# Optimization experiments

Measured on AMD Instinct MI355X. Metric: run time of the kernel, lower is better.

Reference implementation:

```python
import jax, jax.numpy as jnp
import numpy as np

TILE = 16
CLIP_NEAR, CLIP_FAR = 0.01, 10.0


def _sqrt_keepnan(x):
    # forward: sqrt(x) for x>0, NaN otherwise (matches torch.sqrt on negatives);
    # double-where keeps gradients finite.
    pos = x > 0
    return jnp.where(pos, jnp.sqrt(jnp.where(pos, x, 1.0)), jnp.nan)


def _quat_to_rot(q):
    # faithful to the source _quat_to_rot (including its sign quirks)
    x, y, z, w = q[:, 0], q[:, 1], q[:, 2], q[:, 3]
    r0 = jnp.stack([1 - 2 * (y * y + z * z), 2 * (x * y - w * z), 2 * (x * z + w * y)], -1)
    r1 = jnp.stack([2 * (x * y + w * z), 1 - 2 * (x * x - z * z), 2 * (y * z - w * x)], -1)
    r2 = jnp.stack([2 * (x * z + w * y), 2 * (y * z + w * x), 1 - 2 * (x * x + y * y)], -1)
    return jnp.stack([r0, r1, r2], -2)  # (N,3,3)


def _forward(mu, scales, quats, cols, opcs, viewmat, focal, H, W):
    N = mu.shape[0]
    fx = fy = float(focal)
    cx, cy = W / 2.0, H / 2.0
    n_, f_ = CLIP_NEAR, CLIP_FAR

    # --- project gaussians ---
    t = viewmat @ jnp.concatenate([mu.T, jnp.ones((1, N), mu.dtype)], 0)  # (4,N) camera space
    tp0 = (2.0 * fx / W) * t[0]
    tp1 = (2.0 * fy / H) * t[1]
    tp2 = ((f_ + n_) / (f_ - n_)) * t[2] + (-2.0 * f_ * n_ / (f_ - n_)) * t[3]
    tp3 = t[2]
    xys = jnp.stack([W * tp0 / tp3 / 2 + cx, H * tp1 / tp3 / 2 + cy], 1)  # (N,2)
    depths = tp2

    R = _quat_to_rot(quats)
    RS = R * scales[:, None, :]              # R @ diag(s)
    Sigma = RS @ jnp.swapaxes(RS, 1, 2)      # (N,3,3)
    tz = t[2]
    zz = jnp.zeros_like(tz)
    J = jnp.stack([
        jnp.stack([fx / tz, zz, -fx * t[0] / tz ** 2], -1),
        jnp.stack([zz, fy / tz, -fy * t[1] / tz ** 2], -1)], -2)  # (N,2,3)
    Rcw = viewmat[:3, :3]
    M = jnp.einsum('nij,jk->nik', J, Rcw)
    covs = jnp.einsum('nij,njk,nlk->nil', M, Sigma, M)  # (N,2,2)

    ind = jnp.argsort(depths)                # depth sort (front-to-back)
    xys, covs = xys[ind], covs[ind]
    cols_s, opcs_s = cols[ind], opcs[ind]

    # --- bounding boxes -> tile membership mask ---
    a, b, d = covs[:, 0, 0], covs[:, 0, 1], covs[:, 1, 1]
    Aev = jnp.sqrt(a * a - 2 * a * d + 4 * b * b + d * d)
    Bev = a + d
    l1, l2 = 0.5 * (Aev + Bev), 0.5 * (Bev - Aev)
    r1 = 3.0 * _sqrt_keepnan(l1)
    r2 = 3.0 * _sqrt_keepnan(l2)
    mx, my = xys[:, 0], xys[:, 1]
    corners = jnp.stack([
        jnp.stack([mx - r1, my + r2], -1),
        jnp.stack([mx + r1, my + r2], -1),
        jnp.stack([mx + r1, my - r2], -1),
        jnp.stack([mx - r1, my - r2], -1)], 1)  # (N,4,2)
    theta = jnp.where(b != 0, jnp.arctan2(l1 - a, b),
                      jnp.where(a >= d, jnp.pi / 2, 0.0))
    cth, sth = jnp.cos(theta), jnp.sin(theta)
    rot = jnp.stack([jnp.stack([cth, -sth], -1), jnp.stack([sth, cth], -1)], -2)
    bm = corners.mean(1, keepdims=True)
    bbs = jnp.einsum('nij,nkj->nki', rot, corners - bm) + bm
    bbs = jnp.where(jnp.isnan(bbs), -1.0, bbs)
    Wt, Ht = W // TILE, H // TILE
    xmin = jnp.clip(jnp.floor(bbs[:, :, 0].min(1) / TILE), 0, Wt - 1).astype(jnp.int32)
    xmax = jnp.clip(jnp.ceil(bbs[:, :, 0].max(1) / TILE), 0, Wt - 1).astype(jnp.int32)
    ymin = jnp.clip(jnp.floor(bbs[:, :, 1].min(1) / TILE), 0, Ht - 1).astype(jnp.int32)
    ymax = jnp.clip(jnp.ceil(bbs[:, :, 1].max(1) / TILE), 0, Ht - 1).astype(jnp.int32)
    txi = jnp.arange(Wt)
    tyi = jnp.arange(Ht)
    tmask = ((txi[None, None, :] >= xmin[:, None, None]) & (txi[None, None, :] <= xmax[:, None, None]) &
             (tyi[None, :, None] >= ymin[:, None, None]) & (tyi[None, :, None] <= ymax[:, None, None]))  # (N,Ht,Wt)
    pmask = jnp.moveaxis(jnp.repeat(jnp.repeat(tmask, TILE, 1), TILE, 2), 0, -1)  # (H,W,N)

    # --- rasterize: per-pixel gaussian eval + sorted alpha compositing ---
    e = 1e-6
    det = (a + e) * (d + e) - covs[:, 0, 1] * covs[:, 1, 0]
    i00 = (d + e) / det
    i01 = -covs[:, 0, 1] / det
    i10 = -covs[:, 1, 0] / det
    i11 = (a + e) / det
    px = jnp.arange(W, dtype=mu.dtype)
    py = jnp.arange(H, dtype=mu.dtype)
    dx = px[None, :, None] - mx[None, None, :]   # (1,W,N)
    dy = py[:, None, None] - my[None, None, :]   # (H,1,N)
    quad = dx * (i00 * dx + i01 * dy) + dy * (i10 * dx + i11 * dy)  # (H,W,N)
    Pg = jnp.nan_to_num(jnp.exp(-0.5 * quad))
    O = jax.nn.sigmoid(jax.nn.sigmoid(opcs_s))   # double sigmoid: faithful to source
    alpha = O[None, None, :] * Pg
    alpha = jnp.where(pmask, alpha, 0.0)         # only gaussians binned to this tile
    alpha = jnp.where(alpha < 0.001, 0.0, alpha)
    alpha = jnp.minimum(alpha, 0.99)
    trans = jnp.cumprod(1.0 - alpha, -1)         # inclusive transmittance
    Dtr = jnp.concatenate([jnp.ones((H, W, 1), alpha.dtype), trans[..., :-1]], -1)
    C = jnp.clip(cols_s, 1e-4, 1.0)
    rgb = jnp.clip(jnp.einsum('hwn,nc->hwc', alpha * Dtr, C), 1e-4, 1.0)
    nonempty = jnp.repeat(jnp.repeat(tmask.any(0), TILE, 0), TILE, 1)  # empty tiles stay 0
    return jnp.where(nonempty[..., None], rgb, 0.0)


def setup_inputs() -> dict:
    key = jax.random.key(0)
    ks = jax.random.split(key, 6)
    N, H, W = 512, 256, 256
    mu = jax.random.normal(ks[0], (N, 3), jnp.float32)
    scales = jax.random.uniform(ks[1], (N, 3), jnp.float32) * 0.05 + 0.01
    q = jax.random.normal(ks[2], (N, 4), jnp.float32)
    quats = q / jnp.linalg.norm(q, axis=1, keepdims=True)
    cols = jax.random.uniform(ks[3], (N, 3), jnp.float32)
    opcs = jax.random.normal(ks[4], (N,), jnp.float32)
    viewmat = jnp.array([[1, 0, 0, 0], [0, 1, 0, 0], [0, 0, 1, 5.0], [0, 0, 0, 1]], jnp.float32)
    gt = jax.random.uniform(ks[5], (H, W, 3), jnp.float32)
    return {"mu": mu, "scales": scales, "quats": quats, "cols": cols, "opcs": opcs,
            "viewmat": viewmat, "gt": gt, "focal": 200, "H": H, "W": W}


def reference(mu, scales, quats, cols, opcs, viewmat, gt, focal, H, W):
    # gt is accepted (matches source signature) but unused by forward
    return _forward(mu, scales, quats, cols, opcs, viewmat, focal, H, W)
```

## Files before the change

kernel.cpp:

```cpp
#include <hip/hip_runtime.h>
#include <math.h>
#include <float.h>

#define NMAX 512
#define TILE 16
#define FDIV(a,b) __fdividef((a),(b))

__global__ __launch_bounds__(1024) void fused_kernel(
    const float* __restrict__ mu, const float* __restrict__ scales,
    const float* __restrict__ quats, const float* __restrict__ cols,
    const float* __restrict__ opcs, const float* __restrict__ vm,
    const int* __restrict__ focal_p, const int* __restrict__ H_p,
    const int* __restrict__ W_p, float* __restrict__ out, int N)
{
    __shared__ float s_mx[NMAX], s_my[NMAX];
    __shared__ float s_q00[NMAX], s_qs[NMAX], s_q11[NMAX];
    __shared__ float s_O[NMAX], s_c0[NMAX], s_c1[NMAX], s_c2[NMAX];
    __shared__ unsigned long long s_lk[NMAX];
    __shared__ int s_ord[NMAX];
    __shared__ float4 s_part[3][256];
    __shared__ int s_bc[16];

    const int lt = threadIdx.x;
    const int lane = lt & 63, w = lt >> 6;
    const int tx = blockIdx.x, ty = blockIdx.y;

    const int   Wi = W_p[0], Hi = H_p[0];
    const float fx = (float)focal_p[0];
    const float fy = fx;
    const float Wf = (float)Wi, Hf = (float)Hi;
    const float cxf = (float)((double)Wi / 2.0);
    const float cyf = (float)((double)Hi / 2.0);
    const float sxc = (float)(2.0 * (double)fx / (double)Wi);
    const float syc = (float)(2.0 * (double)fy / (double)Hi);
    const float dc1 = (float)((10.0 + 0.01) / (10.0 - 0.01));
    const float dc2 = (float)(-2.0 * 10.0 * 0.01 / (10.0 - 0.01));
    const int Wt = Wi / TILE, Ht = Hi / TILE;

    bool covered = false;
    unsigned int key = 0;
    const int g = lt;
    if (g < N) {
        const float m0 = mu[3*g], m1 = mu[3*g+1], m2 = mu[3*g+2];
        const float t0 = vm[0]*m0  + vm[1]*m1  + vm[2]*m2  + vm[3];
        const float t1 = vm[4]*m0  + vm[5]*m1  + vm[6]*m2  + vm[7];
        const float t2 = vm[8]*m0  + vm[9]*m1  + vm[10]*m2 + vm[11];
        const float t3 = vm[12]*m0 + vm[13]*m1 + vm[14]*m2 + vm[15];

        const float depth = dc1 * t2 + dc2 * t3;
        unsigned int ub = __float_as_uint(depth);
        key = (ub & 0x80000000u) ? ~ub : (ub | 0x80000000u);

        const float mx = FDIV(Wf * (sxc * t0), t2) * 0.5f + cxf;
        const float my = FDIV(Hf * (syc * t1), t2) * 0.5f + cyf;

        const float4 q = ((const float4*)quats)[g];
        const float qx = q.x, qy = q.y, qz = q.z, qw = q.w;
        const float R00 = 1.0f - 2.0f*(qy*qy + qz*qz);
        const float R01 = 2.0f*(qx*qy - qw*qz);
        const float R02 = 2.0f*(qx*qz + qw*qy);
        const float R10 = 2.0f*(qx*qy + qw*qz);
        const float R11 = 1.0f - 2.0f*(qx*qx - qz*qz);
        const float R12 = 2.0f*(qy*qz - qw*qx);
        const float R20 = 2.0f*(qx*qz + qw*qy);
        const float R21 = 2.0f*(qy*qz + qw*qx);
        const float R22 = 1.0f - 2.0f*(qx*qx + qy*qy);

        const float s0 = scales[3*g], s1 = scales[3*g+1], s2 = scales[3*g+2];
        const float A00 = R00*s0, A01 = R01*s1, A02 = R02*s2;
        const float A10 = R10*s0, A11 = R11*s1, A12 = R12*s2;
        const float A20 = R20*s0, A21 = R21*s1, A22 = R22*s2;
        const float S00 = A00*A00 + A01*A01 + A02*A02;
        const float S01 = A00*A10 + A01*A11 + A02*A12;
        const float S02 = A00*A20 + A01*A21 + A02*A22;
        const float S11 = A10*A10 + A11*A11 + A12*A12;
        const float S12 = A10*A20 + A11*A21 + A12*A22;
        const float S22 = A20*A20 + A21*A21 + A22*A22;

        const float tz = t2;
        const float J00 = FDIV(fx, tz);
        const float J02 = FDIV(-fx * t0, tz * tz);
        const float J11 = FDIV(fy, tz);
        const float J12 = FDIV(-fy * t1, tz * tz);
        const float M00 = J00*vm[0] + J02*vm[8];
        const float M01 = J00*vm[1] + J02*vm[9];
        const float M02 = J00*vm[2] + J02*vm[10];
        const float M10 = J11*vm[4] + J12*vm[8];
        const float M11 = J11*vm[5] + J12*vm[9];
        const float M12 = J11*vm[6] + J12*vm[10];
        const float T00 = M00*S00 + M01*S01 + M02*S02;
        const float T01 = M00*S01 + M01*S11 + M02*S12;
        const float T02 = M00*S02 + M01*S12 + M02*S22;
        const float T10 = M10*S00 + M11*S01 + M12*S02;
        const float T11 = M10*S01 + M11*S11 + M12*S12;
        const float T12 = M10*S02 + M11*S12 + M12*S22;
        const float a   = T00*M00 + T01*M01 + T02*M02;
        const float b   = T00*M10 + T01*M11 + T02*M12;
        const float c10 = T10*M00 + T11*M01 + T12*M02;
        const float d   = T10*M10 + T11*M11 + T12*M12;

        const float Aev = sqrtf(a*a - 2.0f*a*d + 4.0f*b*b + d*d);
        const float Bev = a + d;
        const float l1 = 0.5f * (Aev + Bev);
        const float l2 = 0.5f * (Bev - Aev);
        const float r1 = (l1 > 0.0f) ? 3.0f * sqrtf(l1) : NAN;
        const float r2 = (l2 > 0.0f) ? 3.0f * sqrtf(l2) : NAN;

        float cth, sth;
        if (b != 0.0f) {
            const float yv = l1 - a;
            const float h  = sqrtf(b*b + yv*yv);
            cth = FDIV(b,  h);
            sth = FDIV(yv, h);
        } else if (a >= d) {
            cth = -4.371139e-8f;
            sth = 1.0f;
        } else {
            cth = 1.0f;
            sth = 0.0f;
        }

        const float u  = mx - r1, v  = mx + r1;
        const float r_ = my + r2, s_ = my - r2;
        const float bmx = (((u + v) + v) + u) * 0.25f;
        const float bmy = (((r_ + r_) + s_) + s_) * 0.25f;
        const float pxo = u - bmx, qxo = v - bmx;
        const float ryo = r_ - bmy, syo = s_ - bmy;

        const float Axp = cth * pxo, Axq = cth * qxo;
        const float Bxr = (-sth) * ryo, Bxs = (-sth) * syo;
        float xmn  = (fminf(Axp, Axq) + fminf(Bxr, Bxs)) + bmx;
        float xmxv = (fmaxf(Axp, Axq) + fmaxf(Bxr, Bxs)) + bmx;
        const float Ayp = sth * pxo, Ayq = sth * qxo;
        const float Byr = cth * ryo, Bys = cth * syo;
        float ymn  = (fminf(Ayp, Ayq) + fminf(Byr, Bys)) + bmy;
        float ymxv = (fmaxf(Ayp, Ayq) + fmaxf(Byr, Bys)) + bmy;
        if (isnan(xmxv)) { xmn = -1.0f; xmxv = -1.0f; }
        if (isnan(ymxv)) { ymn = -1.0f; ymxv = -1.0f; }

        const int xmin = (int)fminf(fmaxf(floorf(xmn  * 0.0625f), 0.0f), (float)(Wt - 1));
        const int xmax = (int)fminf(fmaxf(ceilf (xmxv * 0.0625f), 0.0f), (float)(Wt - 1));
        const int ymin = (int)fminf(fmaxf(floorf(ymn  * 0.0625f), 0.0f), (float)(Ht - 1));
        const int ymax = (int)fminf(fmaxf(ceilf (ymxv * 0.0625f), 0.0f), (float)(Ht - 1));

        const float e = 1e-06f;
        const float det = (a + e) * (d + e) - b * c10;
        const float idet = FDIV(1.0f, det);

        const float op  = opcs[g];
        const float sg1 = FDIV(1.0f, 1.0f + __expf(-op));

        s_mx [g] = mx;
        s_my [g] = my;
        s_q00[g] = -0.5f * (d + e) * idet;
        s_qs [g] =  0.5f * (b + c10) * idet;
        s_q11[g] = -0.5f * (a + e) * idet;
        s_O  [g] = FDIV(1.0f, 1.0f + __expf(-sg1));
        s_c0 [g] = fminf(fmaxf(cols[3*g    ], 1e-04f), 1.0f);
        s_c1 [g] = fminf(fmaxf(cols[3*g + 1], 1e-04f), 1.0f);
        s_c2 [g] = fminf(fmaxf(cols[3*g + 2], 1e-04f), 1.0f);

        covered = (tx >= xmin) & (tx <= xmax) & (ty >= ymin) & (ty <= ymax);
    }

    const unsigned long long word = __ballot(covered);
    if (lane == 0) s_bc[w] = __popcll(word);
    __syncthreads();

    int base = 0, M = 0;
    #pragma unroll
    for (int i = 0; i < 16; ++i) {
        const int c = s_bc[i];
        if (i < w) base += c;
        M += c;
    }
    if (covered) {
        const int rank = base + __popcll(word & ((1ull << lane) - 1ull));
        s_lk[rank] = ((unsigned long long)key << 32) | (unsigned int)g;
    }
    __syncthreads();

    for (int t = lt; t < M; t += 1024) {
        const unsigned long long mine = s_lk[t];
        int rank = 0;
        for (int s = 0; s < M; ++s) rank += (s_lk[s] < mine) ? 1 : 0;
        s_ord[rank] = (int)(mine & 0xFFFFFFFFu);
    }
    __syncthreads();

    const int p  = lt & 255;
    const int qd = lt >> 8;
    const int W  = gridDim.x * TILE;
    const int px = tx * TILE + (p & 15);
    const int py = ty * TILE + (p >> 4);
    const float fpx = (float)px, fpy = (float)py;

    const int Mq = (M + 3) >> 2;
    const int j0 = qd * Mq;
    const int j1 = min(M, j0 + Mq);

    float Tt = 1.0f, rr = 0.0f, gg = 0.0f, bb = 0.0f;
    for (int j = j0; j < j1; ++j) {
        const int n = s_ord[j];
        const float dx = fpx - s_mx[n];
        const float dy = fpy - s_my[n];
        const float qv = s_q00[n]*dx*dx + s_qs[n]*(dx*dy) + s_q11[n]*dy*dy;
        float Pg = __expf(qv);
        if (Pg != Pg) Pg = 0.0f;
        float alpha = s_O[n] * Pg;
        alpha = (alpha < 0.001f) ? 0.0f : fminf(alpha, 0.99f);
        const float wgt = alpha * Tt;
        rr = fmaf(wgt, s_c0[n], rr);
        gg = fmaf(wgt, s_c1[n], gg);
        bb = fmaf(wgt, s_c2[n], bb);
        Tt = fmaf(-alpha, Tt, Tt);
    }

    if (qd >= 1) s_part[qd - 1][p] = make_float4(rr, gg, bb, Tt);
    __syncthreads();

    if (qd == 0) {
        const float4 q1 = s_part[0][p];
        const float4 q2 = s_part[1][p];
        const float4 q3 = s_part[2][p];
        float cr = fmaf(q2.w, q3.x, q2.x);
        float cg = fmaf(q2.w, q3.y, q2.y);
        float cb = fmaf(q2.w, q3.z, q2.z);
        cr = fmaf(q1.w, cr, q1.x);
        cg = fmaf(q1.w, cg, q1.y);
        cb = fmaf(q1.w, cb, q1.z);
        rr = fmaf(Tt, cr, rr);
        gg = fmaf(Tt, cg, gg);
        bb = fmaf(Tt, cb, bb);

        const int o = (py * W + px) * 3;
        if (M > 0) {
            out[o    ] = fminf(fmaxf(rr, 1e-04f), 1.0f);
            out[o + 1] = fminf(fmaxf(gg, 1e-04f), 1.0f);
            out[o + 2] = fminf(fmaxf(bb, 1e-04f), 1.0f);
        } else {
            out[o] = 0.0f; out[o + 1] = 0.0f; out[o + 2] = 0.0f;
        }
    }
}

extern "C" void kernel_launch(void* const* d_in, const int* in_sizes, int n_in,
                              void* d_out, int out_size, void* d_ws, size_t ws_size,
                              hipStream_t stream) {
    const float* mu     = (const float*)d_in[0];
    const float* scales = (const float*)d_in[1];
    const float* quats  = (const float*)d_in[2];
    const float* cols   = (const float*)d_in[3];
    const float* opcs   = (const float*)d_in[4];
    const float* vm     = (const float*)d_in[5];
    const int* focal_p  = (const int*)d_in[7];
    const int* H_p      = (const int*)d_in[8];
    const int* W_p      = (const int*)d_in[9];

    const int N = in_sizes[4];
    const int HW = out_size / 3;
    int W = (int)(sqrt((double)HW) + 0.5);
    int H = HW / W;

    dim3 grid(W / TILE, H / TILE), block(1024);
    fused_kernel<<<grid, block, 0, stream>>>(mu, scales, quats, cols, opcs, vm,
                                             focal_p, H_p, W_p, (float*)d_out, N);
}
```

Measured before the change: 15.14 us.

## Split per-gaussian projection across both thread halves and factor the 2D covariance

The per-Gaussian preprocessing is split in two. Threads 512-1023, which were idle before, now compute R·diag(s), opacity and colors into shared memory. Threads 0-511 compute the projection and the Jacobian-view product, and after a barrier they form the 2D covariance as B·Bᵀ with B = M·(RS). This replaces the full 3x3 Sigma and the two-step sandwich product, and it uses the symmetric b in place of c10. Divisions are replaced by a single reciprocal of tz and an rsqrt. The change adds a barrier and extra shared memory, and it slightly changes floating-point rounding relative to the reference.

```diff
diff --git a/kernel.cpp b/kernel.cpp
--- a/kernel.cpp
+++ b/kernel.cpp
@@ -16,6 +16,7 @@
     __shared__ float s_mx[NMAX], s_my[NMAX];
     __shared__ float s_q00[NMAX], s_qs[NMAX], s_q11[NMAX];
     __shared__ float s_O[NMAX], s_c0[NMAX], s_c1[NMAX], s_c2[NMAX];
+    __shared__ float4 s_rs0[NMAX], s_rs1[NMAX], s_rs2[NMAX];
     __shared__ unsigned long long s_lk[NMAX];
     __shared__ int s_ord[NMAX];
     __shared__ float4 s_part[3][256];
@@ -39,65 +40,78 @@
 
     bool covered = false;
     unsigned int key = 0;
-    const int g = lt;
-    if (g < N) {
-        const float m0 = mu[3*g], m1 = mu[3*g+1], m2 = mu[3*g+2];
-        const float t0 = vm[0]*m0  + vm[1]*m1  + vm[2]*m2  + vm[3];
-        const float t1 = vm[4]*m0  + vm[5]*m1  + vm[6]*m2  + vm[7];
-        const float t2 = vm[8]*m0  + vm[9]*m1  + vm[10]*m2 + vm[11];
-        const float t3 = vm[12]*m0 + vm[13]*m1 + vm[14]*m2 + vm[15];
-
-        const float depth = dc1 * t2 + dc2 * t3;
-        unsigned int ub = __float_as_uint(depth);
-        key = (ub & 0x80000000u) ? ~ub : (ub | 0x80000000u);
-
-        const float mx = FDIV(Wf * (sxc * t0), t2) * 0.5f + cxf;
-        const float my = FDIV(Hf * (syc * t1), t2) * 0.5f + cyf;
-
-        const float4 q = ((const float4*)quats)[g];
-        const float qx = q.x, qy = q.y, qz = q.z, qw = q.w;
-        const float R00 = 1.0f - 2.0f*(qy*qy + qz*qz);
-        const float R01 = 2.0f*(qx*qy - qw*qz);
-        const float R02 = 2.0f*(qx*qz + qw*qy);
-        const float R10 = 2.0f*(qx*qy + qw*qz);
-        const float R11 = 1.0f - 2.0f*(qx*qx - qz*qz);
-        const float R12 = 2.0f*(qy*qz - qw*qx);
-        const float R20 = 2.0f*(qx*qz + qw*qy);
-        const float R21 = 2.0f*(qy*qz + qw*qx);
-        const float R22 = 1.0f - 2.0f*(qx*qx + qy*qy);
-
-        const float s0 = scales[3*g], s1 = scales[3*g+1], s2 = scales[3*g+2];
-        const float A00 = R00*s0, A01 = R01*s1, A02 = R02*s2;
-        const float A10 = R10*s0, A11 = R11*s1, A12 = R12*s2;
-        const float A20 = R20*s0, A21 = R21*s1, A22 = R22*s2;
-        const float S00 = A00*A00 + A01*A01 + A02*A02;
-        const float S01 = A00*A10 + A01*A11 + A02*A12;
-        const float S02 = A00*A20 + A01*A21 + A02*A22;
-        const float S11 = A10*A10 + A11*A11 + A12*A12;
-        const float S12 = A10*A20 + A11*A21 + A12*A22;
-        const float S22 = A20*A20 + A21*A21 + A22*A22;
-
-        const float tz = t2;
-        const float J00 = FDIV(fx, tz);
-        const float J02 = FDIV(-fx * t0, tz * tz);
-        const float J11 = FDIV(fy, tz);
-        const float J12 = FDIV(-fy * t1, tz * tz);
-        const float M00 = J00*vm[0] + J02*vm[8];
-        const float M01 = J00*vm[1] + J02*vm[9];
-        const float M02 = J00*vm[2] + J02*vm[10];
-        const float M10 = J11*vm[4] + J12*vm[8];
-        const float M11 = J11*vm[5] + J12*vm[9];
-        const float M12 = J11*vm[6] + J12*vm[10];
-        const float T00 = M00*S00 + M01*S01 + M02*S02;
-        const float T01 = M00*S01 + M01*S11 + M02*S12;
-        const float T02 = M00*S02 + M01*S12 + M02*S22;
-        const float T10 = M10*S00 + M11*S01 + M12*S02;
-        const float T11 = M10*S01 + M11*S11 + M12*S12;
-        const float T12 = M10*S02 + M11*S12 + M12*S22;
-        const float a   = T00*M00 + T01*M01 + T02*M02;
-        const float b   = T00*M10 + T01*M11 + T02*M12;
-        const float c10 = T10*M00 + T11*M01 + T12*M02;
-        const float d   = T10*M10 + T11*M11 + T12*M12;
+    float t0, t1, t2, M00, M01, M02, M10, M11, M12, mx, my;
+
+    if (lt >= 512) {
+        const int g2 = lt - 512;
+        if (g2 < N) {
+            const float4 q = ((const float4*)quats)[g2];
+            const float qx = q.x, qy = q.y, qz = q.z, qw = q.w;
+            const float R00 = 1.0f - 2.0f*(qy*qy + qz*qz);
+            const float R01 = 2.0f*(qx*qy - qw*qz);
+            const float R02 = 2.0f*(qx*qz + qw*qy);
+            const float R10 = 2.0f*(qx*qy + qw*qz);
+            const float R11 = 1.0f - 2.0f*(qx*qx - qz*qz);
+            const float R12 = 2.0f*(qy*qz - qw*qx);
+            const float R20 = 2.0f*(qx*qz + qw*qy);
+            const float R21 = 2.0f*(qy*qz + qw*qx);
+            const float R22 = 1.0f - 2.0f*(qx*qx + qy*qy);
+
+            const float s0 = scales[3*g2], s1 = scales[3*g2+1], s2 = scales[3*g2+2];
+            s_rs0[g2] = make_float4(R00*s0, R01*s1, R02*s2, 0.0f);
+            s_rs1[g2] = make_float4(R10*s0, R11*s1, R12*s2, 0.0f);
+            s_rs2[g2] = make_float4(R20*s0, R21*s1, R22*s2, 0.0f);
+
+            const float op  = opcs[g2];
+            const float sg1 = FDIV(1.0f, 1.0f + __expf(-op));
+            s_O [g2] = FDIV(1.0f, 1.0f + __expf(-sg1));
+            s_c0[g2] = fminf(fmaxf(cols[3*g2    ], 1e-04f), 1.0f);
+            s_c1[g2] = fminf(fmaxf(cols[3*g2 + 1], 1e-04f), 1.0f);
+            s_c2[g2] = fminf(fmaxf(cols[3*g2 + 2], 1e-04f), 1.0f);
+        }
+    } else {
+        const int g = lt;
+        if (g < N) {
+            const float m0 = mu[3*g], m1 = mu[3*g+1], m2 = mu[3*g+2];
+            t0 = vm[0]*m0  + vm[1]*m1  + vm[2]*m2  + vm[3];
+            t1 = vm[4]*m0  + vm[5]*m1  + vm[6]*m2  + vm[7];
+            t2 = vm[8]*m0  + vm[9]*m1  + vm[10]*m2 + vm[11];
+            const float t3 = vm[12]*m0 + vm[13]*m1 + vm[14]*m2 + vm[15];
+
+            const float depth = dc1 * t2 + dc2 * t3;
+            unsigned int ub = __float_as_uint(depth);
+            key = (ub & 0x80000000u) ? ~ub : (ub | 0x80000000u);
+
+            const float itz = FDIV(1.0f, t2);
+            mx = (Wf * (sxc * t0)) * itz * 0.5f + cxf;
+            my = (Hf * (syc * t1)) * itz * 0.5f + cyf;
+
+            const float J00 = fx * itz;
+            const float J02 = -fx * t0 * itz * itz;
+            const float J11 = fy * itz;
+            const float J12 = -fy * t1 * itz * itz;
+            M00 = J00*vm[0] + J02*vm[8];
+            M01 = J00*vm[1] + J02*vm[9];
+            M02 = J00*vm[2] + J02*vm[10];
+            M10 = J11*vm[4] + J12*vm[8];
+            M11 = J11*vm[5] + J12*vm[9];
+            M12 = J11*vm[6] + J12*vm[10];
+        }
+    }
+    __syncthreads();
+
+    if (lt < 512 && lt < N) {
+        const int g = lt;
+        const float4 A0 = s_rs0[g], A1 = s_rs1[g], A2 = s_rs2[g];
+        const float B00 = M00*A0.x + M01*A1.x + M02*A2.x;
+        const float B01 = M00*A0.y + M01*A1.y + M02*A2.y;
+        const float B02 = M00*A0.z + M01*A1.z + M02*A2.z;
+        const float B10 = M10*A0.x + M11*A1.x + M12*A2.x;
+        const float B11 = M10*A0.y + M11*A1.y + M12*A2.y;
+        const float B12 = M10*A0.z + M11*A1.z + M12*A2.z;
+        const float a = B00*B00 + B01*B01 + B02*B02;
+        const float b = B00*B10 + B01*B11 + B02*B12;
+        const float d = B10*B10 + B11*B11 + B12*B12;
 
         const float Aev = sqrtf(a*a - 2.0f*a*d + 4.0f*b*b + d*d);
         const float Bev = a + d;
@@ -109,9 +123,9 @@
         float cth, sth;
         if (b != 0.0f) {
             const float yv = l1 - a;
-            const float h  = sqrtf(b*b + yv*yv);
-            cth = FDIV(b,  h);
-            sth = FDIV(yv, h);
+            const float ih = __frsqrt_rn(b*b + yv*yv);
+            cth = b  * ih;
+            sth = yv * ih;
         } else if (a >= d) {
             cth = -4.371139e-8f;
             sth = 1.0f;
@@ -144,21 +158,14 @@
         const int ymax = (int)fminf(fmaxf(ceilf (ymxv * 0.0625f), 0.0f), (float)(Ht - 1));
 
         const float e = 1e-06f;
-        const float det = (a + e) * (d + e) - b * c10;
+        const float det = (a + e) * (d + e) - b * b;
         const float idet = FDIV(1.0f, det);
-
-        const float op  = opcs[g];
-        const float sg1 = FDIV(1.0f, 1.0f + __expf(-op));
 
         s_mx [g] = mx;
         s_my [g] = my;
         s_q00[g] = -0.5f * (d + e) * idet;
-        s_qs [g] =  0.5f * (b + c10) * idet;
+        s_qs [g] = b * idet;
         s_q11[g] = -0.5f * (a + e) * idet;
-        s_O  [g] = FDIV(1.0f, 1.0f + __expf(-sg1));
-        s_c0 [g] = fminf(fmaxf(cols[3*g    ], 1e-04f), 1.0f);
-        s_c1 [g] = fminf(fmaxf(cols[3*g + 1], 1e-04f), 1.0f);
-        s_c2 [g] = fminf(fmaxf(cols[3*g + 2], 1e-04f), 1.0f);
 
         covered = (tx >= xmin) & (tx <= xmax) & (ty >= ymin) & (ty <= ymax);
     }
@@ -176,7 +183,7 @@
     }
     if (covered) {
         const int rank = base + __popcll(word & ((1ull << lane) - 1ull));
-        s_lk[rank] = ((unsigned long long)key << 32) | (unsigned int)g;
+        s_lk[rank] = ((unsigned long long)key << 32) | (unsigned int)lt;
     }
     __syncthreads();
 
```

Measured after the change: 14.63 us. -3.4%, faster.
